# Kernel tuning notes

Measured on AMD Instinct MI355X. Metric: run time of the kernel, lower is better.

The kernel has to match this reference:

```python
import jax, jax.numpy as jnp
import numpy as np
from jax import lax

# dims chosen per init_kwargs / input_specs
B, CIN, H, W = 16, 256, 56, 56
COUT = 256
KH, KW = 3, 3
STRIDE = (1, 1)
PAD = (1, 1)
T = 6          # num_terms
R = 8          # low_rank
KCIN = CIN * KH * KW   # 2304
KR = R * KH * KW       # 72


def setup_inputs() -> dict:
    key = jax.random.key(0)
    k0, k1, k2, k3, k4 = jax.random.split(key, 5)
    x = jax.random.normal(k0, (B, CIN, H, W), dtype=jnp.float32)
    # random sketching matrices (buffers), scaled so U^T U ~ I
    U1s = jax.random.normal(k1, (T, R, COUT), dtype=jnp.float32) / np.float32(np.sqrt(R))
    U2s = jax.random.normal(k2, (T, KR, KCIN), dtype=jnp.float32) / np.float32(np.sqrt(KR))
    # dense kernel [CIN, KH, KW, COUT] (kaiming-ish scale), then build sketched factors
    kernels = jax.random.normal(k3, (CIN, KH, KW, COUT), dtype=jnp.float32) * np.float32(1.0 / np.sqrt(KCIN))
    # S1s[t] = mode4_unfold(kernels @ U1s[t].T) -> [KCIN, R]
    S1s = jnp.einsum('cxyo,tro->tcxyr', kernels, U1s).reshape(T, KCIN, R)
    # S2s[t] = U2s[t] @ K_mat4 -> [KR, COUT]
    K_mat4 = kernels.reshape(KCIN, COUT)
    S2s = jnp.einsum('tqk,ko->tqo', U2s, K_mat4)
    bound = np.float32(1.0 / np.sqrt(KCIN))
    bias = jax.random.uniform(k4, (COUT,), dtype=jnp.float32, minval=-bound, maxval=bound)
    return {"x": x, "S1s": S1s, "S2s": S2s, "U1s": U1s, "U2s": U2s, "bias": bias}


def reference(x, S1s, S2s, U1s, U2s, bias):
    # im2col: patches ordered (c, kh, kw) along the feature axis, matching
    # torch.nn.functional.unfold and the S1s/U2s flattening order.
    patches = lax.conv_general_dilated_patches(
        x, (KH, KW), STRIDE, [(PAD[0], PAD[0]), (PAD[1], PAD[1])])  # [B, KCIN, Ho, Wo]
    Ho, Wo = patches.shape[2], patches.shape[3]
    xw = patches.transpose(0, 2, 3, 1).reshape(-1, KCIN)  # [N, KCIN], N = B*Ho*Wo
    # term 1: (xw @ S1s[t]) @ U1s[t], summed over terms
    y1 = jnp.einsum('tnr,tro->no', jnp.einsum('nk,tkr->tnr', xw, S1s), U1s)
    # term 2: (xw @ U2s[t].T) @ S2s[t], summed over terms
    y2 = jnp.einsum('tnq,tqo->no', jnp.einsum('nk,tqk->tnq', xw, U2s), S2s)
    out = (y1 + y2) / np.float32(2 * T) + bias  # average of 2T unbiased sketch estimates
    return out.reshape(B, Ho, Wo, COUT).transpose(0, 3, 1, 2)  # [B, COUT, Ho, Wo]
```

## Files before the change

kernel.cpp:

```cpp
#include <hip/hip_runtime.h>
#include <hip/hip_bf16.h>

#define B_   16
#define CIN_ 256
#define COUT_ 256
#define HW_  56
#define SP_  3136
#define KCIN_ 2304
#define T_   6
#define R_   8
#define KR_  72

#define WC_ELEMS  (9*256*512)
#define XC_ELEMS  (16*3136*512)
#define ZERO_ELEMS 512

typedef __attribute__((ext_vector_type(4))) float f32x4;
typedef __attribute__((ext_vector_type(8))) short short8;

__device__ __forceinline__ void gld16(const void* g, void* l) {
  __builtin_amdgcn_global_load_lds(
      (const __attribute__((address_space(1))) void*)g,
      (__attribute__((address_space(3))) void*)l, 16, 0, 0);
}

__global__ __launch_bounds__(256) void build_w(
    const float* __restrict__ S1s, const float* __restrict__ S2s,
    const float* __restrict__ U1s, const float* __restrict__ U2s,
    unsigned short* __restrict__ Wc, float* __restrict__ zf)
{
  __shared__ float s1[48];
  __shared__ float u2[432];
  const int k = blockIdx.x;
  const int o = threadIdx.x;
  if (o < 48) { int t = o >> 3, r = o & 7; s1[o] = S1s[t*18432 + k*8 + r]; }
  for (int i = o; i < 432; i += 256) u2[i] = U2s[(size_t)i*2304 + k];
  __syncthreads();
  float acc = 0.f;
  #pragma unroll 8
  for (int i = 0; i < 48; ++i)  acc += s1[i] * U1s[i*256 + o];
  #pragma unroll 8
  for (int i = 0; i < 432; ++i) acc += u2[i] * S2s[i*256 + o];
  acc *= (1.0f/12.0f);
  __hip_bfloat16 h = __float2bfloat16(acc);
  float hv = __bfloat162float(h);
  __hip_bfloat16 l = __float2bfloat16(acc - hv);
  const int c = k / 9, s = k % 9;
  const int base = ((s*256 + o)*8 + (c >> 5))*64 + (c & 31);
  Wc[base]      = *(const unsigned short*)&h;
  Wc[base + 32] = *(const unsigned short*)&l;
  if (k == 0) zf[o] = 0.f;
}

__global__ __launch_bounds__(256) void split_x(
    const float* __restrict__ x, unsigned short* __restrict__ Xc)
{
  const int t  = threadIdx.x;
  const int sp = blockIdx.x*64 + (t >> 2);
  const int cg = blockIdx.y;
  const int b  = blockIdx.z;
  const int c0 = cg*32 + (t & 3)*8;
  const float* src = x + ((size_t)(b*256 + c0))*3136 + sp;
  __align__(16) unsigned short h8[8];
  __align__(16) unsigned short l8[8];
  #pragma unroll
  for (int j = 0; j < 8; ++j) {
    float v = src[(size_t)j*3136];
    __hip_bfloat16 h = __float2bfloat16(v);
    float hv = __bfloat162float(h);
    __hip_bfloat16 l = __float2bfloat16(v - hv);
    h8[j] = *(const unsigned short*)&h;
    l8[j] = *(const unsigned short*)&l;
  }
  unsigned short* dst = Xc + ((size_t)(b*3136 + sp))*512 + cg*64 + (t & 3)*8;
  *(uint4*)dst        = *(const uint4*)h8;
  *(uint4*)(dst + 32) = *(const uint4*)l8;
}

__global__ __launch_bounds__(512, 4) void skconv_gemm(
    const unsigned short* __restrict__ Wc, const unsigned short* __restrict__ Xc,
    const unsigned short* __restrict__ zerobuf, const float* __restrict__ bias,
    float* __restrict__ out)
{
  __shared__ __align__(16) unsigned short lds[20480];
  const int t = threadIdx.x;
  const int lane = t & 63, wid = t >> 6;
  const int blk = blockIdx.x;
  const int b   = blk / 49;
  const int sp0 = (blk % 49) * 64;

  int aoff[4];
  #pragma unroll
  for (int i = 0; i < 4; ++i) {
    int c  = i*512 + t;
    int o  = c >> 3, ph = c & 7;
    aoff[i] = o*512 + ((ph ^ (o & 7)) * 8);
  }
  const int bn   = t >> 3;
  const int bls  = (t & 7) ^ (bn & 7);
  const int bco  = bls * 8;
  const int p    = sp0 + bn;
  const int prow = p / 56, pcol = p % 56;

  const int hs  = ((lane >> 4) ^ (lane & 7)) * 8;
  const int r15 = lane & 15;
  const int wr  = wid >> 1, wcn = wid & 1;
  int ard[4], brd[2];
  #pragma unroll
  for (int mi = 0; mi < 4; ++mi) ard[mi] = (wr*64 + mi*16 + r15)*64 + hs;
  #pragma unroll
  for (int ni = 0; ni < 2; ++ni) brd[ni] = 16384 + (wcn*32 + ni*16 + r15)*64 + hs;

  char* ldsc = (char*)lds;
  char* aDst0 = ldsc + 0*8192  + wid*1024;
  char* aDst1 = ldsc + 1*8192  + wid*1024;
  char* aDst2 = ldsc + 2*8192  + wid*1024;
  char* aDst3 = ldsc + 3*8192  + wid*1024;
  char* bDst  = ldsc + 32768   + wid*1024;

  const f32x4 z4 = {0.f, 0.f, 0.f, 0.f};
  f32x4 acc[4][2];
  #pragma unroll
  for (int mi = 0; mi < 4; ++mi) { acc[mi][0] = z4; acc[mi][1] = z4; }

  #pragma unroll 1
  for (int s = 0; s < 9; ++s) {
    const int kh = s/3 - 1, kw = s%3 - 1;
    const int h2 = prow + kh, w2 = pcol + kw;
    const bool valid = ((unsigned)h2 < 56u) && ((unsigned)w2 < 56u);
    const long long pix = ((long long)(b*3136) + h2*56 + w2)*512 + bco;
    const unsigned short* bs = valid ? (Xc + pix) : zerobuf;
    const unsigned short* as = Wc + s*131072;
    #pragma unroll 1
    for (int c8 = 0; c8 < 8; ++c8) {
      const unsigned short* asc = as + c8*64;
      gld16(asc + aoff[0], aDst0);
      gld16(asc + aoff[1], aDst1);
      gld16(asc + aoff[2], aDst2);
      gld16(asc + aoff[3], aDst3);
      gld16(bs + c8*64,    bDst);
      __syncthreads();
      short8 bh0 = *(const short8*)&lds[brd[0]];
      short8 bh1 = *(const short8*)&lds[brd[1]];
      short8 bl0 = *(const short8*)&lds[brd[0] ^ 32];
      short8 bl1 = *(const short8*)&lds[brd[1] ^ 32];
      #pragma unroll
      for (int mi = 0; mi < 4; ++mi) {
        short8 ah = *(const short8*)&lds[ard[mi]];
        short8 al = *(const short8*)&lds[ard[mi] ^ 32];
        acc[mi][0] = __builtin_amdgcn_mfma_f32_16x16x32_bf16(ah, bh0, acc[mi][0], 0,0,0);
        acc[mi][1] = __builtin_amdgcn_mfma_f32_16x16x32_bf16(ah, bh1, acc[mi][1], 0,0,0);
        acc[mi][0] = __builtin_amdgcn_mfma_f32_16x16x32_bf16(ah, bl0, acc[mi][0], 0,0,0);
        acc[mi][1] = __builtin_amdgcn_mfma_f32_16x16x32_bf16(ah, bl1, acc[mi][1], 0,0,0);
        acc[mi][0] = __builtin_amdgcn_mfma_f32_16x16x32_bf16(al, bh0, acc[mi][0], 0,0,0);
        acc[mi][1] = __builtin_amdgcn_mfma_f32_16x16x32_bf16(al, bh1, acc[mi][1], 0,0,0);
      }
      __syncthreads();
    }
  }

  const int nbase = sp0 + wcn*32 + r15;
  #pragma unroll
  for (int mi = 0; mi < 4; ++mi) {
    const int o0 = wr*64 + mi*16 + ((lane >> 4) << 2);
    float bv[4];
    #pragma unroll
    for (int r = 0; r < 4; ++r) bv[r] = bias[o0 + r];
    #pragma unroll
    for (int ni = 0; ni < 2; ++ni) {
      #pragma unroll
      for (int r = 0; r < 4; ++r) {
        out[((size_t)(b*256 + o0 + r))*3136 + nbase + ni*16] = acc[mi][ni][r] + bv[r];
      }
    }
  }
}

extern "C" void kernel_launch(void* const* d_in, const int* in_sizes, int n_in,
                              void* d_out, int out_size, void* d_ws, size_t ws_size,
                              hipStream_t stream) {
  const float* x    = (const float*)d_in[0];
  const float* S1s  = (const float*)d_in[1];
  const float* S2s  = (const float*)d_in[2];
  const float* U1s  = (const float*)d_in[3];
  const float* U2s  = (const float*)d_in[4];
  const float* bias = (const float*)d_in[5];
  float* out = (float*)d_out;

  unsigned short* Wc = (unsigned short*)d_ws;
  unsigned short* Xc = Wc + WC_ELEMS;
  unsigned short* zb = Xc + XC_ELEMS;

  build_w<<<dim3(2304), dim3(256), 0, stream>>>(S1s, S2s, U1s, U2s, Wc, (float*)zb);
  split_x<<<dim3(49, 8, 16), dim3(256), 0, stream>>>(x, Xc);
  skconv_gemm<<<dim3(784), dim3(512), 0, stream>>>(Wc, Xc, zb, bias, out);
}
```

Baseline: 336.6 us.

## Double-buffer GEMM LDS loads, persistent tiles, and batch build_w over 16 k-columns

The GEMM now uses two LDS buffers so global-to-LDS loads for the next k-step overlap MFMA work on the current one, with explicit vmcnt waits and raw barriers in place of __syncthreads. It becomes a persistent grid of 512 blocks looping over 784 tiles with a swizzled tile order, reordered MFMA issue and setprio. build_w processes 16 k-columns per block, reusing each U1s/S2s load across 16 accumulators instead of one. The costs are doubled LDS per block, which may lower occupancy, and an uneven tail since 784 tiles do not divide evenly over 512 blocks.

```diff
diff --git a/kernel.cpp b/kernel.cpp
--- a/kernel.cpp
+++ b/kernel.cpp
@@ -1,19 +1,12 @@
 #include <hip/hip_runtime.h>
 #include <hip/hip_bf16.h>
 
-#define B_   16
-#define CIN_ 256
-#define COUT_ 256
-#define HW_  56
-#define SP_  3136
-#define KCIN_ 2304
-#define T_   6
-#define R_   8
-#define KR_  72
 
 #define WC_ELEMS  (9*256*512)
 #define XC_ELEMS  (16*3136*512)
-#define ZERO_ELEMS 512
+#define ZB_ELEMS  512
+
+#define BUFSZ 40960
 
 typedef __attribute__((ext_vector_type(4))) float f32x4;
 typedef __attribute__((ext_vector_type(8))) short short8;
@@ -29,27 +22,50 @@
     const float* __restrict__ U1s, const float* __restrict__ U2s,
     unsigned short* __restrict__ Wc, float* __restrict__ zf)
 {
-  __shared__ float s1[48];
-  __shared__ float u2[432];
-  const int k = blockIdx.x;
-  const int o = threadIdx.x;
-  if (o < 48) { int t = o >> 3, r = o & 7; s1[o] = S1s[t*18432 + k*8 + r]; }
-  for (int i = o; i < 432; i += 256) u2[i] = U2s[(size_t)i*2304 + k];
+  __shared__ __align__(16) float tile[480][16];
+  const int tid = threadIdx.x;
+  const int k0 = blockIdx.x * 16;
+  for (int q = tid; q < 192; q += 256) {
+    int tt = q >> 5, rem = q & 31, kk = rem >> 1, rh = rem & 1;
+    float4 v = *(const float4*)&S1s[tt*18432 + (k0+kk)*8 + rh*4];
+    tile[tt*8+rh*4+0][kk] = v.x; tile[tt*8+rh*4+1][kk] = v.y;
+    tile[tt*8+rh*4+2][kk] = v.z; tile[tt*8+rh*4+3][kk] = v.w;
+  }
+  for (int q = tid; q < 1728; q += 256) {
+    int i2 = q >> 2, part = q & 3;
+    float4 v = *(const float4*)&U2s[(size_t)i2*2304 + k0 + part*4];
+    *(float4*)&tile[48+i2][part*4] = v;
+  }
   __syncthreads();
-  float acc = 0.f;
-  #pragma unroll 8
-  for (int i = 0; i < 48; ++i)  acc += s1[i] * U1s[i*256 + o];
-  #pragma unroll 8
-  for (int i = 0; i < 432; ++i) acc += u2[i] * S2s[i*256 + o];
-  acc *= (1.0f/12.0f);
-  __hip_bfloat16 h = __float2bfloat16(acc);
-  float hv = __bfloat162float(h);
-  __hip_bfloat16 l = __float2bfloat16(acc - hv);
-  const int c = k / 9, s = k % 9;
-  const int base = ((s*256 + o)*8 + (c >> 5))*64 + (c & 31);
-  Wc[base]      = *(const unsigned short*)&h;
-  Wc[base + 32] = *(const unsigned short*)&l;
-  if (k == 0) zf[o] = 0.f;
+  const int o = tid;
+  float acc[16];
+  #pragma unroll
+  for (int kk = 0; kk < 16; ++kk) acc[kk] = 0.f;
+  #pragma unroll 4
+  for (int i = 0; i < 48; ++i) {
+    float rv = U1s[i*256 + o];
+    #pragma unroll
+    for (int kk = 0; kk < 16; ++kk) acc[kk] += tile[i][kk] * rv;
+  }
+  #pragma unroll 4
+  for (int i = 0; i < 432; ++i) {
+    float rv = S2s[i*256 + o];
+    #pragma unroll
+    for (int kk = 0; kk < 16; ++kk) acc[kk] += tile[48+i][kk] * rv;
+  }
+  #pragma unroll
+  for (int kk = 0; kk < 16; ++kk) {
+    float a = acc[kk] * (1.0f/12.0f);
+    __hip_bfloat16 h = __float2bfloat16(a);
+    float hv = __bfloat162float(h);
+    __hip_bfloat16 l = __float2bfloat16(a - hv);
+    int k = k0 + kk;
+    int c = k / 9, s = k % 9;
+    int base = s*131072 + o*512 + (c >> 5)*64 + (c & 31);
+    Wc[base]      = *(const unsigned short*)&h;
+    Wc[base + 32] = *(const unsigned short*)&l;
+  }
+  if (blockIdx.x == 0) zf[tid] = 0.f;
 }
 
 __global__ __launch_bounds__(256) void split_x(
@@ -79,98 +95,138 @@
 
 __global__ __launch_bounds__(512, 4) void skconv_gemm(
     const unsigned short* __restrict__ Wc, const unsigned short* __restrict__ Xc,
-    const unsigned short* __restrict__ zerobuf, const float* __restrict__ bias,
+    const unsigned short* __restrict__ zb, const float* __restrict__ bias,
     float* __restrict__ out)
 {
-  __shared__ __align__(16) unsigned short lds[20480];
-  const int t = threadIdx.x;
-  const int lane = t & 63, wid = t >> 6;
-  const int blk = blockIdx.x;
-  const int b   = blk / 49;
-  const int sp0 = (blk % 49) * 64;
-
-  int aoff[4];
-  #pragma unroll
-  for (int i = 0; i < 4; ++i) {
-    int c  = i*512 + t;
-    int o  = c >> 3, ph = c & 7;
-    aoff[i] = o*512 + ((ph ^ (o & 7)) * 8);
-  }
-  const int bn   = t >> 3;
-  const int bls  = (t & 7) ^ (bn & 7);
-  const int bco  = bls * 8;
-  const int p    = sp0 + bn;
-  const int prow = p / 56, pcol = p % 56;
-
-  const int hs  = ((lane >> 4) ^ (lane & 7)) * 8;
-  const int r15 = lane & 15;
-  const int wr  = wid >> 1, wcn = wid & 1;
-  int ard[4], brd[2];
-  #pragma unroll
-  for (int mi = 0; mi < 4; ++mi) ard[mi] = (wr*64 + mi*16 + r15)*64 + hs;
-  #pragma unroll
-  for (int ni = 0; ni < 2; ++ni) brd[ni] = 16384 + (wcn*32 + ni*16 + r15)*64 + hs;
-
-  char* ldsc = (char*)lds;
-  char* aDst0 = ldsc + 0*8192  + wid*1024;
-  char* aDst1 = ldsc + 1*8192  + wid*1024;
-  char* aDst2 = ldsc + 2*8192  + wid*1024;
-  char* aDst3 = ldsc + 3*8192  + wid*1024;
-  char* bDst  = ldsc + 32768   + wid*1024;
+  extern __shared__ __align__(16) char lds[];
+  const int t = threadIdx.x, lane = t & 63, wid = t >> 6;
+
+  int aoff0, aoff1, aoff2, aoff3;
+  {
+    int c, o, ph;
+    c = 0*512 + t; o = c >> 3; ph = c & 7; aoff0 = o*512 + ((ph ^ (o & 7))*8);
+    c = 1*512 + t; o = c >> 3; ph = c & 7; aoff1 = o*512 + ((ph ^ (o & 7))*8);
+    c = 2*512 + t; o = c >> 3; ph = c & 7; aoff2 = o*512 + ((ph ^ (o & 7))*8);
+    c = 3*512 + t; o = c >> 3; ph = c & 7; aoff3 = o*512 + ((ph ^ (o & 7))*8);
+  }
+  const int bn  = t >> 3;
+  const int bco = ((t & 7) ^ (bn & 7)) * 8;
+  const int r15 = lane & 15, kc = lane >> 4;
+  const int hsb = (kc ^ (lane & 7)) * 16;
+  const int wr = wid >> 1, wcn = wid & 1;
+  const int ard0 = (wr*64 +  0 + r15)*128 + hsb;
+  const int ard1 = (wr*64 + 16 + r15)*128 + hsb;
+  const int ard2 = (wr*64 + 32 + r15)*128 + hsb;
+  const int ard3 = (wr*64 + 48 + r15)*128 + hsb;
+  const int brd0 = 32768 + (wcn*32 +  0 + r15)*128 + hsb;
+  const int brd1 = 32768 + (wcn*32 + 16 + r15)*128 + hsb;
+
+  int bb, sp0v, prow, pcol;
+
+  auto STAGE = [&](int bufb, int step) {
+    const int s = step >> 3, c8 = step & 7;
+    const unsigned short* as = Wc + s*131072 + c8*64;
+    char* base = lds + bufb + wid*1024;
+    gld16(as + aoff0, base);
+    gld16(as + aoff1, base + 8192);
+    gld16(as + aoff2, base + 16384);
+    gld16(as + aoff3, base + 24576);
+    const int kh = s/3 - 1, kw = s%3 - 1;
+    const int h2 = prow + kh, w2 = pcol + kw;
+    const bool valid = ((unsigned)h2 < 56u) & ((unsigned)w2 < 56u);
+    const unsigned short* bsrc = valid
+        ? Xc + ((size_t)(bb*3136 + h2*56 + w2))*512 + c8*64 + bco
+        : zb + c8*64 + bco;
+    gld16(bsrc, base + 32768);
+  };
 
   const f32x4 z4 = {0.f, 0.f, 0.f, 0.f};
   f32x4 acc[4][2];
-  #pragma unroll
-  for (int mi = 0; mi < 4; ++mi) { acc[mi][0] = z4; acc[mi][1] = z4; }
+
+  auto COMPUTE = [&](int bufb) {
+    const char* L = lds + bufb;
+    short8 bh0 = *(const short8*)(L + brd0);
+    short8 bh1 = *(const short8*)(L + brd1);
+    short8 bl0 = *(const short8*)(L + (brd0 ^ 64));
+    short8 bl1 = *(const short8*)(L + (brd1 ^ 64));
+    short8 ah0 = *(const short8*)(L + ard0);
+    short8 ah1 = *(const short8*)(L + ard1);
+    short8 ah2 = *(const short8*)(L + ard2);
+    short8 ah3 = *(const short8*)(L + ard3);
+    short8 al0 = *(const short8*)(L + (ard0 ^ 64));
+    short8 al1 = *(const short8*)(L + (ard1 ^ 64));
+    short8 al2 = *(const short8*)(L + (ard2 ^ 64));
+    short8 al3 = *(const short8*)(L + (ard3 ^ 64));
+    asm volatile("s_waitcnt lgkmcnt(0)" ::: "memory");
+    __builtin_amdgcn_sched_barrier(0);
+    __builtin_amdgcn_s_setprio(1);
+    acc[0][0] = __builtin_amdgcn_mfma_f32_16x16x32_bf16(ah0, bh0, acc[0][0], 0,0,0);
+    acc[0][1] = __builtin_amdgcn_mfma_f32_16x16x32_bf16(ah0, bh1, acc[0][1], 0,0,0);
+    acc[1][0] = __builtin_amdgcn_mfma_f32_16x16x32_bf16(ah1, bh0, acc[1][0], 0,0,0);
+    acc[1][1] = __builtin_amdgcn_mfma_f32_16x16x32_bf16(ah1, bh1, acc[1][1], 0,0,0);
+    acc[2][0] = __builtin_amdgcn_mfma_f32_16x16x32_bf16(ah2, bh0, acc[2][0], 0,0,0);
+    acc[2][1] = __builtin_amdgcn_mfma_f32_16x16x32_bf16(ah2, bh1, acc[2][1], 0,0,0);
+    acc[3][0] = __builtin_amdgcn_mfma_f32_16x16x32_bf16(ah3, bh0, acc[3][0], 0,0,0);
+    acc[3][1] = __builtin_amdgcn_mfma_f32_16x16x32_bf16(ah3, bh1, acc[3][1], 0,0,0);
+    acc[0][0] = __builtin_amdgcn_mfma_f32_16x16x32_bf16(ah0, bl0, acc[0][0], 0,0,0);
+    acc[0][1] = __builtin_amdgcn_mfma_f32_16x16x32_bf16(ah0, bl1, acc[0][1], 0,0,0);
+    acc[1][0] = __builtin_amdgcn_mfma_f32_16x16x32_bf16(ah1, bl0, acc[1][0], 0,0,0);
+    acc[1][1] = __builtin_amdgcn_mfma_f32_16x16x32_bf16(ah1, bl1, acc[1][1], 0,0,0);
+    acc[2][0] = __builtin_amdgcn_mfma_f32_16x16x32_bf16(ah2, bl0, acc[2][0], 0,0,0);
+    acc[2][1] = __builtin_amdgcn_mfma_f32_16x16x32_bf16(ah2, bl1, acc[2][1], 0,0,0);
+    acc[3][0] = __builtin_amdgcn_mfma_f32_16x16x32_bf16(ah3, bl0, acc[3][0], 0,0,0);
+    acc[3][1] = __builtin_amdgcn_mfma_f32_16x16x32_bf16(ah3, bl1, acc[3][1], 0,0,0);
+    acc[0][0] = __builtin_amdgcn_mfma_f32_16x16x32_bf16(al0, bh0, acc[0][0], 0,0,0);
+    acc[0][1] = __builtin_amdgcn_mfma_f32_16x16x32_bf16(al0, bh1, acc[0][1], 0,0,0);
+    acc[1][0] = __builtin_amdgcn_mfma_f32_16x16x32_bf16(al1, bh0, acc[1][0], 0,0,0);
+    acc[1][1] = __builtin_amdgcn_mfma_f32_16x16x32_bf16(al1, bh1, acc[1][1], 0,0,0);
+    acc[2][0] = __builtin_amdgcn_mfma_f32_16x16x32_bf16(al2, bh0, acc[2][0], 0,0,0);
+    acc[2][1] = __builtin_amdgcn_mfma_f32_16x16x32_bf16(al2, bh1, acc[2][1], 0,0,0);
+    acc[3][0] = __builtin_amdgcn_mfma_f32_16x16x32_bf16(al3, bh0, acc[3][0], 0,0,0);
+    acc[3][1] = __builtin_amdgcn_mfma_f32_16x16x32_bf16(al3, bh1, acc[3][1], 0,0,0);
+    __builtin_amdgcn_s_setprio(0);
+  };
 
   #pragma unroll 1
-  for (int s = 0; s < 9; ++s) {
-    const int kh = s/3 - 1, kw = s%3 - 1;
-    const int h2 = prow + kh, w2 = pcol + kw;
-    const bool valid = ((unsigned)h2 < 56u) && ((unsigned)w2 < 56u);
-    const long long pix = ((long long)(b*3136) + h2*56 + w2)*512 + bco;
-    const unsigned short* bs = valid ? (Xc + pix) : zerobuf;
-    const unsigned short* as = Wc + s*131072;
+  for (int tv = blockIdx.x; tv < 784; tv += 512) {
+    const int tile = (tv & 7)*98 + (tv >> 3);
+    bb = tile / 49; sp0v = (tile % 49) * 64;
+    const int p = sp0v + bn; prow = p / 56; pcol = p % 56;
+    #pragma unroll
+    for (int mi = 0; mi < 4; ++mi) { acc[mi][0] = z4; acc[mi][1] = z4; }
+
+    STAGE(0, 0);
     #pragma unroll 1
-    for (int c8 = 0; c8 < 8; ++c8) {
-      const unsigned short* asc = as + c8*64;
-      gld16(asc + aoff[0], aDst0);
-      gld16(asc + aoff[1], aDst1);
-      gld16(asc + aoff[2], aDst2);
-      gld16(asc + aoff[3], aDst3);
-      gld16(bs + c8*64,    bDst);
-      __syncthreads();
-      short8 bh0 = *(const short8*)&lds[brd[0]];
-      short8 bh1 = *(const short8*)&lds[brd[1]];
-      short8 bl0 = *(const short8*)&lds[brd[0] ^ 32];
-      short8 bl1 = *(const short8*)&lds[brd[1] ^ 32];
+    for (int step = 0; step < 72; step += 2) {
+      STAGE(BUFSZ, step + 1);
+      asm volatile("s_waitcnt vmcnt(5)" ::: "memory");
+      __builtin_amdgcn_s_barrier();
+      COMPUTE(0);
+      __builtin_amdgcn_s_barrier();
+      if (step + 2 < 72) {
+        STAGE(0, step + 2);
+        asm volatile("s_waitcnt vmcnt(5)" ::: "memory");
+      } else {
+        asm volatile("s_waitcnt vmcnt(0)" ::: "memory");
+      }
+      __builtin_amdgcn_s_barrier();
+      COMPUTE(BUFSZ);
+      __builtin_amdgcn_s_barrier();
+    }
+
+    const int nbase = sp0v + wcn*32 + r15;
+    #pragma unroll
+    for (int mi = 0; mi < 4; ++mi) {
+      const int o0 = wr*64 + mi*16 + kc*4;
+      float4 bv = *(const float4*)&bias[o0];
+      const float bvr[4] = {bv.x, bv.y, bv.z, bv.w};
       #pragma unroll
-      for (int mi = 0; mi < 4; ++mi) {
-        short8 ah = *(const short8*)&lds[ard[mi]];
-        short8 al = *(const short8*)&lds[ard[mi] ^ 32];
-        acc[mi][0] = __builtin_amdgcn_mfma_f32_16x16x32_bf16(ah, bh0, acc[mi][0], 0,0,0);
-        acc[mi][1] = __builtin_amdgcn_mfma_f32_16x16x32_bf16(ah, bh1, acc[mi][1], 0,0,0);
-        acc[mi][0] = __builtin_amdgcn_mfma_f32_16x16x32_bf16(ah, bl0, acc[mi][0], 0,0,0);
-        acc[mi][1] = __builtin_amdgcn_mfma_f32_16x16x32_bf16(ah, bl1, acc[mi][1], 0,0,0);
-        acc[mi][0] = __builtin_amdgcn_mfma_f32_16x16x32_bf16(al, bh0, acc[mi][0], 0,0,0);
-        acc[mi][1] = __builtin_amdgcn_mfma_f32_16x16x32_bf16(al, bh1, acc[mi][1], 0,0,0);
-      }
-      __syncthreads();
-    }
-  }
-
-  const int nbase = sp0 + wcn*32 + r15;
-  #pragma unroll
-  for (int mi = 0; mi < 4; ++mi) {
-    const int o0 = wr*64 + mi*16 + ((lane >> 4) << 2);
-    float bv[4];
-    #pragma unroll
-    for (int r = 0; r < 4; ++r) bv[r] = bias[o0 + r];
-    #pragma unroll
-    for (int ni = 0; ni < 2; ++ni) {
-      #pragma unroll
-      for (int r = 0; r < 4; ++r) {
-        out[((size_t)(b*256 + o0 + r))*3136 + nbase + ni*16] = acc[mi][ni][r] + bv[r];
+      for (int ni = 0; ni < 2; ++ni) {
+        #pragma unroll
+        for (int r = 0; r < 4; ++r) {
+          out[((size_t)(bb*256 + o0 + r))*3136 + nbase + ni*16]
+              = acc[mi][ni][r] + bvr[r];
+        }
       }
     }
   }
@@ -189,9 +245,12 @@
 
   unsigned short* Wc = (unsigned short*)d_ws;
   unsigned short* Xc = Wc + WC_ELEMS;
-  unsigned short* zb = Xc + XC_ELEMS;
-
-  build_w<<<dim3(2304), dim3(256), 0, stream>>>(S1s, S2s, U1s, U2s, Wc, (float*)zb);
+  unsigned short* zbuf = Xc + XC_ELEMS;
+
+  (void)hipFuncSetAttribute(reinterpret_cast<const void*>(skconv_gemm),
+                            hipFuncAttributeMaxDynamicSharedMemorySize, 2*BUFSZ);
+
+  build_w<<<dim3(144), dim3(256), 0, stream>>>(S1s, S2s, U1s, U2s, Wc, (float*)zbuf);
   split_x<<<dim3(49, 8, 16), dim3(256), 0, stream>>>(x, Xc);
-  skconv_gemm<<<dim3(784), dim3(512), 0, stream>>>(Wc, Xc, zb, bias, out);
-}
+  skconv_gemm<<<dim3(512), dim3(512), 2*BUFSZ, stream>>>(Wc, Xc, zbuf, bias, out);
+}
```

Result: faster. 319.8 us (-5.0%).
